# Optimization experiments

Hardware: AMD Instinct MI355X
Metric: run time of the kernel (lower is better)

## Reference

```python
import jax, jax.numpy as jnp
import numpy as np

C = 128
ATTN_DIM = C // 8   # 16
VALUE_DIM = C // 2  # 64

def _xavier(key, shape):
    # xavier_uniform for torch Linear weight (out,in); we store transposed (in,out)
    fan_in, fan_out = shape[0], shape[1]
    a = jnp.sqrt(6.0 / (fan_in + fan_out))
    return jax.random.uniform(key, shape, jnp.float32, -a, a)

def setup_inputs() -> dict:
    key = jax.random.key(0)
    ks = jax.random.split(key, 5)
    x = jax.random.normal(ks[0], (8, C, 64, 64), jnp.float32)
    return {
        "x": x,
        "Wq": _xavier(ks[1], (C, ATTN_DIM)),  "bq": jnp.zeros((ATTN_DIM,), jnp.float32),
        "Wk": _xavier(ks[2], (C, ATTN_DIM)),  "bk": jnp.zeros((ATTN_DIM,), jnp.float32),
        "Wv": _xavier(ks[3], (C, VALUE_DIM)), "bv": jnp.zeros((VALUE_DIM,), jnp.float32),
        "Wo": _xavier(ks[4], (VALUE_DIM, C)), "bo": jnp.zeros((C,), jnp.float32),
        "gamma": jnp.ones((), jnp.float32),
    }

def _maxpool2x2(t):
    # t: (N, D, H, W) -> (N, D, H//2, W//2), MaxPool2d((2,2), stride=2)
    N, D, H, W = t.shape
    return t.reshape(N, D, H // 2, 2, W // 2, 2).max(axis=(3, 5))

def reference(x, Wq, bq, Wk, bk, Wv, bv, Wo, bo, gamma):
    N, Cc, H, W = x.shape
    xf = x.reshape(N, Cc, H * W).transpose(0, 2, 1)          # (N, HW, C)
    q = xf @ Wq + bq                                          # (N, HW, d)
    k = (xf @ Wk + bk).reshape(N, H, W, ATTN_DIM).transpose(0, 3, 1, 2)
    k = _maxpool2x2(k).reshape(N, ATTN_DIM, -1)               # (N, d, HW/4)
    scores = jnp.einsum('bqd,bdk->bqk', q, k)                 # (N, HW, HW/4)
    attn = jax.nn.softmax(scores, axis=-1)
    v = (xf @ Wv + bv).reshape(N, H, W, VALUE_DIM).transpose(0, 3, 1, 2)
    v = _maxpool2x2(v).reshape(N, VALUE_DIM, -1).transpose(0, 2, 1)  # (N, HW/4, dv)
    ao = jnp.einsum('bqk,bkv->bqv', attn, v)                  # (N, HW, dv)
    out = (ao @ Wo + bo).reshape(N, H, W, Cc).transpose(0, 3, 1, 2)
    return x + gamma * out
```

## Files before the change

### kernel.cpp

```cpp
#include <hip/hip_runtime.h>
#include <cstddef>

#define CC   128
#define AD   16
#define VD   64
#define HWN  4096
#define PJ   1024
#define NB   8

typedef short short8 __attribute__((ext_vector_type(8)));
typedef float f32x4  __attribute__((ext_vector_type(4)));
typedef unsigned short u16;

__device__ inline u16 f2bf(float f) {
    union { float f; unsigned u; } a; a.f = f;
    unsigned r = a.u + 0x7fff + ((a.u >> 16) & 1);
    return (u16)(r >> 16);
}
__device__ inline float bf16f(u16 v) {
    union { unsigned u; float f; } a; a.u = ((unsigned)v) << 16;
    return a.f;
}

__device__ inline int ph128(int r, int c) { return r * 128 + ((((c >> 3) ^ (r & 7)) << 3) | (c & 7)); }
__device__ inline int ph64 (int r, int c) { return r * 64  + ((((c >> 3) ^ (r & 7)) << 3) | (c & 7)); }

__global__ __launch_bounds__(256) void k_proj(
    const float* __restrict__ x,
    const float* __restrict__ Wq, const float* __restrict__ bq,
    const float* __restrict__ Wk, const float* __restrict__ bk,
    const float* __restrict__ Wv, const float* __restrict__ bv,
    u16* __restrict__ Qp, u16* __restrict__ Kp, u16* __restrict__ Vt)
{
    __shared__ __align__(16) u16 xT[128 * 128];
    __shared__ __align__(16) u16 WT[96 * 128];

    const int tile = blockIdx.x, n = blockIdx.y, t = threadIdx.x;
    const int p0 = tile * 128;
    const int l = t & 63, w = t >> 6, g = l >> 4, lm = l & 15;

    {
        const float* xb = x + (size_t)n * CC * HWN + p0;
#pragma unroll
        for (int it = 0; it < 16; ++it) {
            const int idx = t + 256 * it;
            const int p4 = idx & 31, ch = idx >> 5;
            const float4 v = *(const float4*)(xb + (size_t)ch * HWN + p4 * 4);
            xT[ph128(p4 * 4 + 0, ch)] = f2bf(v.x);
            xT[ph128(p4 * 4 + 1, ch)] = f2bf(v.y);
            xT[ph128(p4 * 4 + 2, ch)] = f2bf(v.z);
            xT[ph128(p4 * 4 + 3, ch)] = f2bf(v.w);
        }
    }
#pragma unroll
    for (int it = 0; it < 2; ++it) {
        const int idx = t + 256 * it;
        const int d4 = idx & 3, ch = idx >> 2;
        float4 v = *(const float4*)(Wq + ch * AD + d4 * 4);
        WT[ph128(d4 * 4 + 0, ch)] = f2bf(v.x);
        WT[ph128(d4 * 4 + 1, ch)] = f2bf(v.y);
        WT[ph128(d4 * 4 + 2, ch)] = f2bf(v.z);
        WT[ph128(d4 * 4 + 3, ch)] = f2bf(v.w);
        v = *(const float4*)(Wk + ch * AD + d4 * 4);
        WT[ph128(16 + d4 * 4 + 0, ch)] = f2bf(v.x);
        WT[ph128(16 + d4 * 4 + 1, ch)] = f2bf(v.y);
        WT[ph128(16 + d4 * 4 + 2, ch)] = f2bf(v.z);
        WT[ph128(16 + d4 * 4 + 3, ch)] = f2bf(v.w);
    }
#pragma unroll
    for (int it = 0; it < 8; ++it) {
        const int idx = t + 256 * it;
        const int d4 = idx & 15, ch = idx >> 4;
        const float4 v = *(const float4*)(Wv + ch * VD + d4 * 4);
        WT[ph128(32 + d4 * 4 + 0, ch)] = f2bf(v.x);
        WT[ph128(32 + d4 * 4 + 1, ch)] = f2bf(v.y);
        WT[ph128(32 + d4 * 4 + 2, ch)] = f2bf(v.z);
        WT[ph128(32 + d4 * 4 + 3, ch)] = f2bf(v.w);
    }
    __syncthreads();

    f32x4 acc[2][6];
#pragma unroll
    for (int i = 0; i < 2; ++i)
#pragma unroll
        for (int j = 0; j < 6; ++j) acc[i][j] = (f32x4){0.f, 0.f, 0.f, 0.f};
#pragma unroll
    for (int ks = 0; ks < 4; ++ks) {
        const short8 a0 = *(const short8*)&xT[ph128((w * 2 + 0) * 16 + lm, ks * 32 + g * 8)];
        const short8 a1 = *(const short8*)&xT[ph128((w * 2 + 1) * 16 + lm, ks * 32 + g * 8)];
#pragma unroll
        for (int nt = 0; nt < 6; ++nt) {
            const short8 b = *(const short8*)&WT[ph128(nt * 16 + lm, ks * 32 + g * 8)];
            acc[0][nt] = __builtin_amdgcn_mfma_f32_16x16x32_bf16(a0, b, acc[0][nt], 0, 0, 0);
            acc[1][nt] = __builtin_amdgcn_mfma_f32_16x16x32_bf16(a1, b, acc[1][nt], 0, 0, 0);
        }
    }
    __syncthreads();
#pragma unroll
    for (int mt = 0; mt < 2; ++mt)
#pragma unroll
        for (int nt = 0; nt < 6; ++nt)
#pragma unroll
            for (int r = 0; r < 4; ++r)
                xT[ph128((w * 2 + mt) * 16 + g * 4 + r, nt * 16 + lm)] = f2bf(acc[mt][nt][r]);
    __syncthreads();

    {
        const int pos = t >> 1, half = t & 1;
        const short8 s = *(const short8*)&xT[ph128(pos, half * 8)];
        u16 res[8];
#pragma unroll
        for (int j = 0; j < 8; ++j)
            res[j] = f2bf(bf16f((u16)s[j]) + bq[half * 8 + j]);
        *(uint4*)(Qp + (size_t)(n * HWN + p0 + pos) * AD + half * 8) = *(const uint4*)res;
    }
#pragma unroll
    for (int it = 0; it < 2; ++it) {
        const int idx = t + 256 * it;
        const int c2 = idx >> 4, d = idx & 15;
        const float m = fmaxf(
            fmaxf(bf16f(xT[ph128(2 * c2,      16 + d)]), bf16f(xT[ph128(2 * c2 + 1,  16 + d)])),
            fmaxf(bf16f(xT[ph128(64 + 2 * c2, 16 + d)]), bf16f(xT[ph128(65 + 2 * c2, 16 + d)])));
        Kp[(size_t)(n * PJ + tile * 32 + c2) * AD + d] = f2bf(m + bk[d]);
    }
    {
        const int dv = t >> 2, seg = t & 3;
        u16 res[8];
#pragma unroll
        for (int i = 0; i < 8; ++i) {
            const int c2 = seg * 8 + i;
            const float m = fmaxf(
                fmaxf(bf16f(xT[ph128(2 * c2,      32 + dv)]), bf16f(xT[ph128(2 * c2 + 1,  32 + dv)])),
                fmaxf(bf16f(xT[ph128(64 + 2 * c2, 32 + dv)]), bf16f(xT[ph128(65 + 2 * c2, 32 + dv)])));
            res[i] = f2bf(m + bv[dv]);
        }
        *(uint4*)(Vt + (size_t)(n * VD + dv) * PJ + tile * 32 + seg * 8) = *(const uint4*)res;
    }
}

__global__ __launch_bounds__(256) void k_attn(
    const float* __restrict__ x,
    const u16* __restrict__ Qp, const u16* __restrict__ Kp, const u16* __restrict__ Vt,
    const float* __restrict__ Wo, const float* __restrict__ bo,
    const float* __restrict__ gma,
    float* __restrict__ out)
{
    __shared__ __align__(16) u16 smemA[128 * 16 + 64 * 128];
    __shared__ __align__(16) u16 smemB[4 * 16 * 128];

    const int n = blockIdx.y, t = threadIdx.x;
    const int q0b = blockIdx.x * 64;
    const int l = t & 63, w = t >> 6, g = l >> 4, lm = l & 15;

    u16* Kl = smemA;
    u16* Vl = smemA + 2048;
    u16* Pl = smemB + w * 2048;

    short8 qf = {0, 0, 0, 0, 0, 0, 0, 0};
    if (g < 2)
        qf = *(const short8*)(Qp + (size_t)(n * HWN + q0b + w * 16 + lm) * AD + g * 8);

    f32x4 O[4];
#pragma unroll
    for (int i = 0; i < 4; ++i) O[i] = (f32x4){0.f, 0.f, 0.f, 0.f};
    float mr[4] = {-1e30f, -1e30f, -1e30f, -1e30f};
    float lr[4] = {0.f, 0.f, 0.f, 0.f};

    for (int ch = 0; ch < 8; ++ch) {
        const int j0 = ch * 128;
        __syncthreads();
        {
            const int j = t >> 1, half = t & 1;
            const uint4 v = *(const uint4*)(Kp + (size_t)(n * PJ + j0 + j) * AD + half * 8);
            *(uint4*)&Kl[(j * 2 + (half ^ (j & 1))) * 8] = v;
        }
        {
            const int dv = t >> 2, seg = t & 3;
            const u16* src = Vt + (size_t)(n * VD + dv) * PJ + j0;
#pragma unroll
            for (int i = 0; i < 4; ++i) {
                const int jb = seg * 4 + i;
                const uint4 v = *(const uint4*)(src + jb * 8);
                *(uint4*)&Vl[(dv * 16 + (jb ^ (dv & 7))) * 8] = v;
            }
        }
        __syncthreads();

        f32x4 S[8];
#pragma unroll
        for (int jt = 0; jt < 8; ++jt) {
            short8 kb = {0, 0, 0, 0, 0, 0, 0, 0};
            if (g < 2) {
                const int j = jt * 16 + lm;
                kb = *(const short8*)&Kl[(j * 2 + (g ^ (j & 1))) * 8];
            }
            const f32x4 z = (f32x4){0.f, 0.f, 0.f, 0.f};
            S[jt] = __builtin_amdgcn_mfma_f32_16x16x32_bf16(qf, kb, z, 0, 0, 0);
        }

#pragma unroll
        for (int r = 0; r < 4; ++r) {
            float cm = S[0][r];
#pragma unroll
            for (int jt = 1; jt < 8; ++jt) cm = fmaxf(cm, S[jt][r]);
            cm = fmaxf(cm, __shfl_xor(cm, 1));
            cm = fmaxf(cm, __shfl_xor(cm, 2));
            cm = fmaxf(cm, __shfl_xor(cm, 4));
            cm = fmaxf(cm, __shfl_xor(cm, 8));
            const float nm = fmaxf(mr[r], cm);
            const float al = __expf(mr[r] - nm);
            mr[r] = nm;
            const int row = g * 4 + r;
            float sum = 0.f;
#pragma unroll
            for (int jt = 0; jt < 8; ++jt) {
                const float p = __expf(S[jt][r] - nm);
                sum += p;
                Pl[ph128(row, jt * 16 + lm)] = f2bf(p);
            }
            sum += __shfl_xor(sum, 1);
            sum += __shfl_xor(sum, 2);
            sum += __shfl_xor(sum, 4);
            sum += __shfl_xor(sum, 8);
            lr[r] = lr[r] * al + sum;
            O[0][r] *= al; O[1][r] *= al; O[2][r] *= al; O[3][r] *= al;
        }

#pragma unroll
        for (int ks = 0; ks < 4; ++ks) {
            const short8 pf = *(const short8*)&Pl[ph128(lm, ks * 32 + g * 8)];
#pragma unroll
            for (int dt = 0; dt < 4; ++dt) {
                const short8 vf = *(const short8*)&Vl[ph128(dt * 16 + lm, ks * 32 + g * 8)];
                O[dt] = __builtin_amdgcn_mfma_f32_16x16x32_bf16(pf, vf, O[dt], 0, 0, 0);
            }
        }
    }

    u16* Ol = smemB + w * 2048;
#pragma unroll
    for (int r = 0; r < 4; ++r) {
        const float inv = 1.f / lr[r];
        const int row = g * 4 + r;
#pragma unroll
        for (int dt = 0; dt < 4; ++dt)
            Ol[ph64(row, dt * 16 + lm)] = f2bf(O[dt][r] * inv);
    }
    __syncthreads();
#pragma unroll
    for (int it = 0; it < 8; ++it) {
        const int idx = t + 256 * it;
        const int c4 = idx & 31, dv = idx >> 5;
        const float4 v = *(const float4*)(Wo + dv * CC + c4 * 4);
        smemA[ph64(c4 * 4 + 0, dv)] = f2bf(v.x);
        smemA[ph64(c4 * 4 + 1, dv)] = f2bf(v.y);
        smemA[ph64(c4 * 4 + 2, dv)] = f2bf(v.z);
        smemA[ph64(c4 * 4 + 3, dv)] = f2bf(v.w);
    }
    __syncthreads();

    const float gm = gma[0];
#pragma unroll
    for (int mt = 0; mt < 8; ++mt) {
        f32x4 D = (f32x4){0.f, 0.f, 0.f, 0.f};
#pragma unroll
        for (int ks = 0; ks < 2; ++ks) {
            const short8 af = *(const short8*)&smemA[ph64(mt * 16 + lm, ks * 32 + g * 8)];
            const short8 bf = *(const short8*)&Ol[ph64(lm, ks * 32 + g * 8)];
            D = __builtin_amdgcn_mfma_f32_16x16x32_bf16(af, bf, D, 0, 0, 0);
        }
#pragma unroll
        for (int r = 0; r < 4; ++r) {
            const int c = mt * 16 + g * 4 + r;
            const size_t off = ((size_t)n * CC + c) * HWN + q0b + w * 16 + lm;
            out[off] = x[off] + gm * (D[r] + bo[c]);
        }
    }
}

extern "C" void kernel_launch(void* const* d_in, const int* in_sizes, int n_in,
                              void* d_out, int out_size, void* d_ws, size_t ws_size,
                              hipStream_t stream) {
    const float* x     = (const float*)d_in[0];
    const float* Wq    = (const float*)d_in[1];
    const float* bq    = (const float*)d_in[2];
    const float* Wk    = (const float*)d_in[3];
    const float* bk    = (const float*)d_in[4];
    const float* Wv    = (const float*)d_in[5];
    const float* bv    = (const float*)d_in[6];
    const float* Wo    = (const float*)d_in[7];
    const float* bo    = (const float*)d_in[8];
    const float* gamma = (const float*)d_in[9];
    float* out = (float*)d_out;

    u16* Qp = (u16*)d_ws;
    u16* Kp = Qp + (size_t)NB * HWN * AD;
    u16* Vt = Kp + (size_t)NB * PJ * AD;

    k_proj<<<dim3(32, NB), 256, 0, stream>>>(x, Wq, bq, Wk, bk, Wv, bv, Qp, Kp, Vt);
    k_attn<<<dim3(64, NB), 256, 0, stream>>>(x, Qp, Kp, Vt, Wo, bo, gamma, out);
}
```

Baseline: 122.0 us.

## Double-buffer K/V via direct global-to-LDS loads and pool projections in registers

```diff
diff --git a/kernel.cpp b/kernel.cpp
--- a/kernel.cpp
+++ b/kernel.cpp
@@ -1,5 +1,7 @@
 #include <hip/hip_runtime.h>
+#include <hip/hip_bf16.h>
 #include <cstddef>
+#include <cstdint>
 
 #define CC   128
 #define AD   16
@@ -13,9 +15,12 @@
 typedef unsigned short u16;
 
 __device__ inline u16 f2bf(float f) {
-    union { float f; unsigned u; } a; a.f = f;
-    unsigned r = a.u + 0x7fff + ((a.u >> 16) & 1);
-    return (u16)(r >> 16);
+    __hip_bfloat16 h = __float2bfloat16(f);
+    union { __hip_bfloat16 h; u16 u; } c; c.h = h; return c.u;
+}
+__device__ inline unsigned pk2(float a, float b) {
+    __hip_bfloat162 h = __float22bfloat162_rn(make_float2(a, b));
+    union { __hip_bfloat162 h; unsigned u; } c; c.h = h; return c.u;
 }
 __device__ inline float bf16f(u16 v) {
     union { unsigned u; float f; } a; a.u = ((unsigned)v) << 16;
@@ -24,13 +29,23 @@
 
 __device__ inline int ph128(int r, int c) { return r * 128 + ((((c >> 3) ^ (r & 7)) << 3) | (c & 7)); }
 __device__ inline int ph64 (int r, int c) { return r * 64  + ((((c >> 3) ^ (r & 7)) << 3) | (c & 7)); }
+
+__device__ inline void stage16(const u16* g, u16* l) {
+#if __has_builtin(__builtin_amdgcn_global_load_lds)
+    __builtin_amdgcn_global_load_lds(
+        (const __attribute__((address_space(1))) unsigned int*)g,
+        (__attribute__((address_space(3))) unsigned int*)l, 16, 0, 0);
+#else
+    *(uint4*)l = *(const uint4*)g;
+#endif
+}
 
 __global__ __launch_bounds__(256) void k_proj(
     const float* __restrict__ x,
     const float* __restrict__ Wq, const float* __restrict__ bq,
     const float* __restrict__ Wk, const float* __restrict__ bk,
     const float* __restrict__ Wv, const float* __restrict__ bv,
-    u16* __restrict__ Qp, u16* __restrict__ Kp, u16* __restrict__ Vt)
+    u16* __restrict__ Qp, u16* __restrict__ Kp, u16* __restrict__ Vt2)
 {
     __shared__ __align__(16) u16 xT[128 * 128];
     __shared__ __align__(16) u16 WT[96 * 128];
@@ -42,14 +57,22 @@
     {
         const float* xb = x + (size_t)n * CC * HWN + p0;
 #pragma unroll
-        for (int it = 0; it < 16; ++it) {
+        for (int it = 0; it < 4; ++it) {
             const int idx = t + 256 * it;
-            const int p4 = idx & 31, ch = idx >> 5;
-            const float4 v = *(const float4*)(xb + (size_t)ch * HWN + p4 * 4);
-            xT[ph128(p4 * 4 + 0, ch)] = f2bf(v.x);
-            xT[ph128(p4 * 4 + 1, ch)] = f2bf(v.y);
-            xT[ph128(p4 * 4 + 2, ch)] = f2bf(v.z);
-            xT[ph128(p4 * 4 + 3, ch)] = f2bf(v.w);
+            const int p4 = idx & 31, c4 = idx >> 5;
+            const float* bp = xb + p4 * 4;
+            const f32x4 r0 = *(const f32x4*)(bp + (size_t)(c4 * 4 + 0) * HWN);
+            const f32x4 r1 = *(const f32x4*)(bp + (size_t)(c4 * 4 + 1) * HWN);
+            const f32x4 r2 = *(const f32x4*)(bp + (size_t)(c4 * 4 + 2) * HWN);
+            const f32x4 r3 = *(const f32x4*)(bp + (size_t)(c4 * 4 + 3) * HWN);
+#pragma unroll
+            for (int pp = 0; pp < 4; ++pp) {
+                const int pos = p4 * 4 + pp;
+                uint2 v;
+                v.x = pk2(r0[pp], r1[pp]);
+                v.y = pk2(r2[pp], r3[pp]);
+                *(uint2*)&xT[pos * 128 + ((((c4 >> 1) ^ (pos & 7)) << 3) | ((c4 & 1) * 4))] = v;
+            }
         }
     }
 #pragma unroll
@@ -86,8 +109,8 @@
         for (int j = 0; j < 6; ++j) acc[i][j] = (f32x4){0.f, 0.f, 0.f, 0.f};
 #pragma unroll
     for (int ks = 0; ks < 4; ++ks) {
-        const short8 a0 = *(const short8*)&xT[ph128((w * 2 + 0) * 16 + lm, ks * 32 + g * 8)];
-        const short8 a1 = *(const short8*)&xT[ph128((w * 2 + 1) * 16 + lm, ks * 32 + g * 8)];
+        const short8 a0 = *(const short8*)&xT[ph128(w * 16 + lm,       ks * 32 + g * 8)];
+        const short8 a1 = *(const short8*)&xT[ph128((w + 4) * 16 + lm, ks * 32 + g * 8)];
 #pragma unroll
         for (int nt = 0; nt < 6; ++nt) {
             const short8 b = *(const short8*)&WT[ph128(nt * 16 + lm, ks * 32 + g * 8)];
@@ -95,96 +118,96 @@
             acc[1][nt] = __builtin_amdgcn_mfma_f32_16x16x32_bf16(a1, b, acc[1][nt], 0, 0, 0);
         }
     }
-    __syncthreads();
-#pragma unroll
-    for (int mt = 0; mt < 2; ++mt)
-#pragma unroll
-        for (int nt = 0; nt < 6; ++nt)
-#pragma unroll
-            for (int r = 0; r < 4; ++r)
-                xT[ph128((w * 2 + mt) * 16 + g * 4 + r, nt * 16 + lm)] = f2bf(acc[mt][nt][r]);
-    __syncthreads();
-
-    {
-        const int pos = t >> 1, half = t & 1;
-        const short8 s = *(const short8*)&xT[ph128(pos, half * 8)];
-        u16 res[8];
-#pragma unroll
-        for (int j = 0; j < 8; ++j)
-            res[j] = f2bf(bf16f((u16)s[j]) + bq[half * 8 + j]);
-        *(uint4*)(Qp + (size_t)(n * HWN + p0 + pos) * AD + half * 8) = *(const uint4*)res;
-    }
-#pragma unroll
-    for (int it = 0; it < 2; ++it) {
-        const int idx = t + 256 * it;
-        const int c2 = idx >> 4, d = idx & 15;
-        const float m = fmaxf(
-            fmaxf(bf16f(xT[ph128(2 * c2,      16 + d)]), bf16f(xT[ph128(2 * c2 + 1,  16 + d)])),
-            fmaxf(bf16f(xT[ph128(64 + 2 * c2, 16 + d)]), bf16f(xT[ph128(65 + 2 * c2, 16 + d)])));
-        Kp[(size_t)(n * PJ + tile * 32 + c2) * AD + d] = f2bf(m + bk[d]);
-    }
-    {
-        const int dv = t >> 2, seg = t & 3;
-        u16 res[8];
-#pragma unroll
-        for (int i = 0; i < 8; ++i) {
-            const int c2 = seg * 8 + i;
-            const float m = fmaxf(
-                fmaxf(bf16f(xT[ph128(2 * c2,      32 + dv)]), bf16f(xT[ph128(2 * c2 + 1,  32 + dv)])),
-                fmaxf(bf16f(xT[ph128(64 + 2 * c2, 32 + dv)]), bf16f(xT[ph128(65 + 2 * c2, 32 + dv)])));
-            res[i] = f2bf(m + bv[dv]);
-        }
-        *(uint4*)(Vt + (size_t)(n * VD + dv) * PJ + tile * 32 + seg * 8) = *(const uint4*)res;
+
+    const float bqv = bq[lm], bkv = bk[lm];
+
+#pragma unroll
+    for (int mi = 0; mi < 2; ++mi) {
+        const int mt = w + mi * 4;
+#pragma unroll
+        for (int r = 0; r < 4; ++r) {
+            const int pos = mt * 16 + g * 4 + r;
+            Qp[((size_t)n * HWN + p0 + pos) * AD + lm] = f2bf(acc[mi][0][r] + bqv);
+        }
+    }
+#pragma unroll
+    for (int a = 0; a < 2; ++a) {
+        const float m = fmaxf(fmaxf(acc[0][1][2 * a], acc[0][1][2 * a + 1]),
+                              fmaxf(acc[1][1][2 * a], acc[1][1][2 * a + 1])) + bkv;
+        const int j = tile * 32 + w * 8 + g * 2 + a;
+        const int dsw = (((lm >> 3) ^ (j & 1)) << 3) | (lm & 7);
+        Kp[((size_t)n * PJ + j) * AD + dsw] = f2bf(m);
+    }
+#pragma unroll
+    for (int nt = 0; nt < 4; ++nt) {
+        const int dv = nt * 16 + lm;
+        const float bvv = bv[dv];
+        const float m0 = fmaxf(fmaxf(acc[0][nt + 2][0], acc[0][nt + 2][1]),
+                               fmaxf(acc[1][nt + 2][0], acc[1][nt + 2][1])) + bvv;
+        const float m1 = fmaxf(fmaxf(acc[0][nt + 2][2], acc[0][nt + 2][3]),
+                               fmaxf(acc[1][nt + 2][2], acc[1][nt + 2][3])) + bvv;
+        const int jl  = (tile & 3) * 32 + w * 8 + g * 2;
+        const int jsw = (((jl >> 3) ^ (dv & 7)) << 3) | (jl & 7);
+        *(unsigned*)&Vt2[((((size_t)n * 8 + (tile >> 2)) * VD + dv) << 7) + jsw] = pk2(m0, m1);
     }
 }
 
 __global__ __launch_bounds__(256) void k_attn(
     const float* __restrict__ x,
-    const u16* __restrict__ Qp, const u16* __restrict__ Kp, const u16* __restrict__ Vt,
+    const u16* __restrict__ Qp, const u16* __restrict__ Kp, const u16* __restrict__ Vt2,
     const float* __restrict__ Wo, const float* __restrict__ bo,
     const float* __restrict__ gma,
     float* __restrict__ out)
 {
-    __shared__ __align__(16) u16 smemA[128 * 16 + 64 * 128];
-    __shared__ __align__(16) u16 smemB[4 * 16 * 128];
+    __shared__ __align__(16) u16 KV[2][10240];
+    __shared__ __align__(16) u16 PB[4 * 2048];
 
     const int n = blockIdx.y, t = threadIdx.x;
     const int q0b = blockIdx.x * 64;
     const int l = t & 63, w = t >> 6, g = l >> 4, lm = l & 15;
 
-    u16* Kl = smemA;
-    u16* Vl = smemA + 2048;
-    u16* Pl = smemB + w * 2048;
-
     short8 qf = {0, 0, 0, 0, 0, 0, 0, 0};
     if (g < 2)
-        qf = *(const short8*)(Qp + (size_t)(n * HWN + q0b + w * 16 + lm) * AD + g * 8);
+        qf = *(const short8*)(Qp + ((size_t)n * HWN + q0b + w * 16 + lm) * AD + g * 8);
+
+    float xr[8][4];
+#pragma unroll
+    for (int mt = 0; mt < 8; ++mt)
+#pragma unroll
+        for (int r = 0; r < 4; ++r)
+            xr[mt][r] = x[((size_t)n * CC + mt * 16 + g * 4 + r) * HWN + q0b + w * 16 + lm];
+
+    const u16* Kg = Kp  + (size_t)n * PJ * AD;
+    const u16* Vg = Vt2 + (size_t)n * 8 * VD * 128;
+
+    {
+        stage16(Kg + t * 8, &KV[0][t * 8]);
+#pragma unroll
+        for (int i = 0; i < 4; ++i)
+            stage16(Vg + ((w * 4 + i) * 64 + l) * 8, &KV[0][2048 + (w * 4 + i) * 512 + l * 8]);
+    }
+    __syncthreads();
 
     f32x4 O[4];
 #pragma unroll
     for (int i = 0; i < 4; ++i) O[i] = (f32x4){0.f, 0.f, 0.f, 0.f};
     float mr[4] = {-1e30f, -1e30f, -1e30f, -1e30f};
     float lr[4] = {0.f, 0.f, 0.f, 0.f};
+    u16* Pl = PB + w * 2048;
 
     for (int ch = 0; ch < 8; ++ch) {
-        const int j0 = ch * 128;
-        __syncthreads();
-        {
-            const int j = t >> 1, half = t & 1;
-            const uint4 v = *(const uint4*)(Kp + (size_t)(n * PJ + j0 + j) * AD + half * 8);
-            *(uint4*)&Kl[(j * 2 + (half ^ (j & 1))) * 8] = v;
-        }
-        {
-            const int dv = t >> 2, seg = t & 3;
-            const u16* src = Vt + (size_t)(n * VD + dv) * PJ + j0;
-#pragma unroll
-            for (int i = 0; i < 4; ++i) {
-                const int jb = seg * 4 + i;
-                const uint4 v = *(const uint4*)(src + jb * 8);
-                *(uint4*)&Vl[(dv * 16 + (jb ^ (dv & 7))) * 8] = v;
-            }
-        }
-        __syncthreads();
+        const u16* Kl = KV[ch & 1];
+        const u16* Vl = KV[ch & 1] + 2048;
+
+        if (ch < 7) {
+            const int b = (ch + 1) & 1;
+            const size_t ko = (size_t)(ch + 1) * 2048, vo = (size_t)(ch + 1) * 8192;
+            stage16(Kg + ko + t * 8, &KV[b][t * 8]);
+#pragma unroll
+            for (int i = 0; i < 4; ++i)
+                stage16(Vg + vo + ((w * 4 + i) * 64 + l) * 8,
+                        &KV[b][2048 + (w * 4 + i) * 512 + l * 8]);
+        }
 
         f32x4 S[8];
 #pragma unroll
@@ -235,9 +258,10 @@
                 O[dt] = __builtin_amdgcn_mfma_f32_16x16x32_bf16(pf, vf, O[dt], 0, 0, 0);
             }
         }
-    }
-
-    u16* Ol = smemB + w * 2048;
+        __syncthreads();
+    }
+
+    u16* Ol = Pl;
 #pragma unroll
     for (int r = 0; r < 4; ++r) {
         const float inv = 1.f / lr[r];
@@ -246,16 +270,16 @@
         for (int dt = 0; dt < 4; ++dt)
             Ol[ph64(row, dt * 16 + lm)] = f2bf(O[dt][r] * inv);
     }
-    __syncthreads();
+    u16* WoTl = (u16*)KV;
 #pragma unroll
     for (int it = 0; it < 8; ++it) {
         const int idx = t + 256 * it;
         const int c4 = idx & 31, dv = idx >> 5;
         const float4 v = *(const float4*)(Wo + dv * CC + c4 * 4);
-        smemA[ph64(c4 * 4 + 0, dv)] = f2bf(v.x);
-        smemA[ph64(c4 * 4 + 1, dv)] = f2bf(v.y);
-        smemA[ph64(c4 * 4 + 2, dv)] = f2bf(v.z);
-        smemA[ph64(c4 * 4 + 3, dv)] = f2bf(v.w);
+        WoTl[ph64(c4 * 4 + 0, dv)] = f2bf(v.x);
+        WoTl[ph64(c4 * 4 + 1, dv)] = f2bf(v.y);
+        WoTl[ph64(c4 * 4 + 2, dv)] = f2bf(v.z);
+        WoTl[ph64(c4 * 4 + 3, dv)] = f2bf(v.w);
     }
     __syncthreads();
 
@@ -265,7 +289,7 @@
         f32x4 D = (f32x4){0.f, 0.f, 0.f, 0.f};
 #pragma unroll
         for (int ks = 0; ks < 2; ++ks) {
-            const short8 af = *(const short8*)&smemA[ph64(mt * 16 + lm, ks * 32 + g * 8)];
+            const short8 af = *(const short8*)&WoTl[ph64(mt * 16 + lm, ks * 32 + g * 8)];
             const short8 bf = *(const short8*)&Ol[ph64(lm, ks * 32 + g * 8)];
             D = __builtin_amdgcn_mfma_f32_16x16x32_bf16(af, bf, D, 0, 0, 0);
         }
@@ -273,7 +297,7 @@
         for (int r = 0; r < 4; ++r) {
             const int c = mt * 16 + g * 4 + r;
             const size_t off = ((size_t)n * CC + c) * HWN + q0b + w * 16 + lm;
-            out[off] = x[off] + gm * (D[r] + bo[c]);
+            out[off] = xr[mt][r] + gm * (D[r] + bo[c]);
         }
     }
 }
@@ -293,10 +317,10 @@
     const float* gamma = (const float*)d_in[9];
     float* out = (float*)d_out;
 
-    u16* Qp = (u16*)d_ws;
-    u16* Kp = Qp + (size_t)NB * HWN * AD;
-    u16* Vt = Kp + (size_t)NB * PJ * AD;
-
-    k_proj<<<dim3(32, NB), 256, 0, stream>>>(x, Wq, bq, Wk, bk, Wv, bv, Qp, Kp, Vt);
-    k_attn<<<dim3(64, NB), 256, 0, stream>>>(x, Qp, Kp, Vt, Wo, bo, gamma, out);
-}
+    u16* Qp  = (u16*)d_ws;
+    u16* Kp  = Qp + (size_t)NB * HWN * AD;
+    u16* Vt2 = Kp + (size_t)NB * PJ * AD;
+
+    k_proj<<<dim3(32, NB), 256, 0, stream>>>(x, Wq, bq, Wk, bk, Wv, bv, Qp, Kp, Vt2);
+    k_attn<<<dim3(64, NB), 256, 0, stream>>>(x, Qp, Kp, Vt2, Wo, bo, gamma, out);
+}
```

After: 122.0 us. No clear change (+0.0%).
